# Performance work log

Hardware: AMD Instinct MI355X
Metric: run time of the kernel (lower is better)

The kernel has to match this reference:

```python
import jax, jax.numpy as jnp
import numpy as np

D_MODEL, N_HEADS, D_FF = 1024, 16, 4096
D_HEAD = D_MODEL // N_HEADS
B, S = 2, 2048
EPS = 1e-5


def setup_inputs() -> dict:
    key = jax.random.key(0)
    ks = jax.random.split(key, 12)
    sd = 1.0 / np.sqrt(D_MODEL)
    return {
        "x": jax.random.normal(ks[0], (B, S, D_MODEL), jnp.float32),
        "relative_bias": jax.random.normal(ks[1], (1, N_HEADS, S, S), jnp.float32),
        # attention projections, stored as (in, out) so y = x @ W
        "wq": jax.random.normal(ks[2], (D_MODEL, D_MODEL), jnp.float32) * sd,
        "wk": jax.random.normal(ks[3], (D_MODEL, D_MODEL), jnp.float32) * sd,
        "wv": jax.random.normal(ks[4], (D_MODEL, D_MODEL), jnp.float32) * sd,
        "wo": jax.random.normal(ks[5], (D_MODEL, D_MODEL), jnp.float32) * sd,
        "wo_b": jnp.zeros((D_MODEL,), jnp.float32),
        # FFN
        "w1": jax.random.normal(ks[6], (D_MODEL, D_FF), jnp.float32) * sd,
        "b1": jnp.zeros((D_FF,), jnp.float32),
        "w2": jax.random.normal(ks[7], (D_FF, D_MODEL), jnp.float32) * (1.0 / np.sqrt(D_FF)),
        "b2": jnp.zeros((D_MODEL,), jnp.float32),
        # LayerNorms
        "ln1_g": jnp.ones((D_MODEL,), jnp.float32),
        "ln1_b": jnp.zeros((D_MODEL,), jnp.float32),
        "ln2_g": jnp.ones((D_MODEL,), jnp.float32),
        "ln2_b": jnp.zeros((D_MODEL,), jnp.float32),
    }


def _layernorm(x, g, b):
    mu = jnp.mean(x, axis=-1, keepdims=True)
    var = jnp.mean(jnp.square(x - mu), axis=-1, keepdims=True)
    return (x - mu) * jax.lax.rsqrt(var + EPS) * g + b


def _attn(x, relative_bias, wq, wk, wv, wo, wo_b):
    b, s, d = x.shape
    # (B,S,D) -> (B,H,S,Dh)
    def split_heads(t):
        return t.reshape(b, s, N_HEADS, D_HEAD).transpose(0, 2, 1, 3)
    q = split_heads(x @ wq)
    k = split_heads(x @ wk)
    v = split_heads(x @ wv)
    scores = jnp.einsum("bhqd,bhkd->bhqk", q, k) / np.sqrt(D_HEAD) + relative_bias
    attn = jax.nn.softmax(scores, axis=-1)
    ctx = jnp.einsum("bhqk,bhkd->bhqd", attn, v)
    ctx = ctx.transpose(0, 2, 1, 3).reshape(b, s, d)
    return ctx @ wo + wo_b


def _ffn(x, w1, b1, w2, b2):
    return jax.nn.gelu(x @ w1 + b1, approximate=False) @ w2 + b2


def reference(x, relative_bias, wq, wk, wv, wo, wo_b, w1, b1, w2, b2,
              ln1_g, ln1_b, ln2_g, ln2_b):
    x = x + _attn(_layernorm(x, ln1_g, ln1_b), relative_bias, wq, wk, wv, wo, wo_b)
    x = x + _ffn(_layernorm(x, ln2_g, ln2_b), w1, b1, w2, b2)
    return x
```

## Files before the change

### kernel.cpp

```cpp
#include <hip/hip_runtime.h>
#include <hip/hip_bf16.h>
#include <stdint.h>

typedef unsigned short u16;
typedef __bf16 bf16x8 __attribute__((ext_vector_type(8)));
typedef u16   u16x8  __attribute__((ext_vector_type(8)));
typedef u16   u16x4  __attribute__((ext_vector_type(4)));
typedef float f32x4  __attribute__((ext_vector_type(4)));

__device__ __forceinline__ u16 f2bf(float f) {
  union { float f; uint32_t u; } v; v.f = f;
  uint32_t r = v.u + 0x7fffu + ((v.u >> 16) & 1u);
  return (u16)(r >> 16);
}

typedef __attribute__((address_space(1))) void gvoid_t;
typedef __attribute__((address_space(3))) void lvoid_t;
__device__ __forceinline__ void gload_lds16(const void* g, void* l) {
  __builtin_amdgcn_global_load_lds((gvoid_t*)g, (lvoid_t*)l, 16, 0, 0);
}

__global__ __launch_bounds__(256)
void ln_kernel(const float* __restrict__ x, const float* __restrict__ g,
               const float* __restrict__ b, u16* __restrict__ out) {
  const int row = blockIdx.x;
  const int tid = threadIdx.x;
  const float* xr = x + (size_t)row * 1024;
  f32x4 v = *(const f32x4*)&xr[tid * 4];
  float s = v[0] + v[1] + v[2] + v[3];
  float q = v[0]*v[0] + v[1]*v[1] + v[2]*v[2] + v[3]*v[3];
  #pragma unroll
  for (int o = 32; o > 0; o >>= 1) { s += __shfl_xor(s, o); q += __shfl_xor(q, o); }
  __shared__ float ss[4], qq[4];
  if ((tid & 63) == 0) { ss[tid >> 6] = s; qq[tid >> 6] = q; }
  __syncthreads();
  s = ss[0] + ss[1] + ss[2] + ss[3];
  q = qq[0] + qq[1] + qq[2] + qq[3];
  float mu = s * (1.0f / 1024.0f);
  float var = q * (1.0f / 1024.0f) - mu * mu;
  float rstd = rsqrtf(var + 1e-5f);
  u16x4 o4;
  #pragma unroll
  for (int i = 0; i < 4; ++i)
    o4[i] = f2bf((v[i] - mu) * rstd * g[tid * 4 + i] + b[tid * 4 + i]);
  *(u16x4*)&out[(size_t)row * 1024 + tid * 4] = o4;
}

__global__ __launch_bounds__(256)
void transpose_cast(const float* __restrict__ W, u16* __restrict__ Wt, int K, int N) {
  __shared__ float t[32][33];
  const int n0 = blockIdx.x * 32, k0 = blockIdx.y * 32;
  const int tx = threadIdx.x & 31, ty = threadIdx.x >> 5;
  #pragma unroll
  for (int i = 0; i < 4; ++i)
    t[ty + 8*i][tx] = W[(size_t)(k0 + ty + 8*i) * N + n0 + tx];
  __syncthreads();
  #pragma unroll
  for (int i = 0; i < 4; ++i)
    Wt[(size_t)(n0 + ty + 8*i) * K + k0 + tx] = f2bf(t[tx][ty + 8*i]);
}

template<int EPI>
__global__ __launch_bounds__(256, 2)
void gemm_bt(const u16* __restrict__ A, const u16* __restrict__ Bt,
             void* __restrict__ out, const float* __restrict__ bias,
             const float* __restrict__ resid, int M, int N, int K) {
  __shared__ u16 As[128 * 32];
  __shared__ u16 Bs[128 * 32];
  const int tid = threadIdx.x;
  const int w = tid >> 6, l = tid & 63;
  const int bm = blockIdx.x * 128, bn = blockIdx.y * 128;
  const int wr = (w >> 1) * 64, wc = (w & 1) * 64;
  const int l15 = l & 15, lhi = l >> 4;
  f32x4 acc[4][4] = {};

  const int r4 = tid >> 2;
  const int c8 = (tid & 3) * 8;
  const u16* ga0 = A  + (size_t)(bm + r4) * K + c8;
  const u16* ga1 = ga0 + (size_t)64 * K;
  const u16* gb0 = Bt + (size_t)(bn + r4) * K + c8;
  const u16* gb1 = gb0 + (size_t)64 * K;
  u16* lA0 = &As[(w * 16) * 32];
  u16* lA1 = &As[(64 + w * 16) * 32];
  u16* lB0 = &Bs[(w * 16) * 32];
  u16* lB1 = &Bs[(64 + w * 16) * 32];

  const int arow = (wr + l15) * 32 + lhi * 8;
  const int brow = (wc + l15) * 32 + lhi * 8;

  for (int k0 = 0; k0 < K; k0 += 32) {
    gload_lds16(ga0 + k0, lA0);
    gload_lds16(ga1 + k0, lA1);
    gload_lds16(gb0 + k0, lB0);
    gload_lds16(gb1 + k0, lB1);
    __syncthreads();
    bf16x8 a[4], b[4];
    #pragma unroll
    for (int m = 0; m < 4; ++m) a[m] = *(const bf16x8*)&As[arow + m * 16 * 32];
    #pragma unroll
    for (int n = 0; n < 4; ++n) b[n] = *(const bf16x8*)&Bs[brow + n * 16 * 32];
    #pragma unroll
    for (int m = 0; m < 4; ++m)
      #pragma unroll
      for (int n = 0; n < 4; ++n)
        acc[m][n] = __builtin_amdgcn_mfma_f32_16x16x32_bf16(a[m], b[n], acc[m][n], 0, 0, 0);
    __syncthreads();
  }

  #pragma unroll
  for (int m = 0; m < 4; ++m) {
    #pragma unroll
    for (int n = 0; n < 4; ++n) {
      #pragma unroll
      for (int r = 0; r < 4; ++r) {
        const int grow = bm + wr + m * 16 + lhi * 4 + r;
        const int gcol = bn + wc + n * 16 + l15;
        float vv = acc[m][n][r];
        if constexpr (EPI >= 1) vv += bias[gcol];
        if constexpr (EPI == 1) vv = 0.5f * vv * (1.0f + erff(vv * 0.70710678118f));
        if constexpr (EPI == 2) {
          vv += resid[(size_t)grow * N + gcol];
          ((float*)out)[(size_t)grow * N + gcol] = vv;
        } else {
          ((u16*)out)[(size_t)grow * N + gcol] = f2bf(vv);
        }
      }
    }
  }
}

__global__ __launch_bounds__(256, 2)
void attn_kernel(const u16* __restrict__ qkv, const float* __restrict__ bias,
                 u16* __restrict__ ctx) {
  const int qt = blockIdx.x;
  const int bh = blockIdx.y;
  const int b = bh >> 4, h = bh & 15;
  const int tid = threadIdx.x, w = tid >> 6, l = tid & 63;
  const int l15 = l & 15, lhi = l >> 4;
  const size_t ld = 3072;

  __shared__ u16 Kl[64 * 72];
  __shared__ u16 Vt[64 * 72];
  __shared__ u16 Pl[4][16 * 72];

  const u16* qp = qkv;
  const u16* kp = qkv + 1024;
  const u16* vp = qkv + 2048;

  bf16x8 qf[2];
  {
    const u16* qrow = qp + (size_t)(b * 2048 + qt * 64 + w * 16 + l15) * ld + h * 64 + lhi * 8;
    qf[0] = *(const bf16x8*)qrow;
    qf[1] = *(const bf16x8*)(qrow + 32);
  }

  float m_run[4] = {-1e30f, -1e30f, -1e30f, -1e30f};
  float s_run[4] = {0.f, 0.f, 0.f, 0.f};
  f32x4 octx[4] = {};

  const int key = tid & 63, dh = (tid >> 6) * 16;
  const u16* kgl = kp + (size_t)(b * 2048 + key) * ld + h * 64 + dh;
  const u16* vgl = vp + (size_t)(b * 2048 + key) * ld + h * 64 + dh;

  for (int kv0 = 0; kv0 < 2048; kv0 += 64) {
    u16x8 k0v = *(const u16x8*)(kgl + (size_t)kv0 * ld);
    u16x8 k1v = *(const u16x8*)(kgl + (size_t)kv0 * ld + 8);
    u16x8 v0v = *(const u16x8*)(vgl + (size_t)kv0 * ld);
    u16x8 v1v = *(const u16x8*)(vgl + (size_t)kv0 * ld + 8);
    *(u16x8*)&Kl[key * 72 + dh] = k0v;
    *(u16x8*)&Kl[key * 72 + dh + 8] = k1v;
    #pragma unroll
    for (int i = 0; i < 8; ++i) {
      Vt[(dh + i) * 72 + key]     = v0v[i];
      Vt[(dh + 8 + i) * 72 + key] = v1v[i];
    }
    __syncthreads();

    f32x4 sa[4] = {};
    #pragma unroll
    for (int nf = 0; nf < 4; ++nf) {
      bf16x8 kf0 = *(const bf16x8*)&Kl[(nf * 16 + l15) * 72 + lhi * 8];
      bf16x8 kf1 = *(const bf16x8*)&Kl[(nf * 16 + l15) * 72 + 32 + lhi * 8];
      sa[nf] = __builtin_amdgcn_mfma_f32_16x16x32_bf16(qf[0], kf0, sa[nf], 0, 0, 0);
      sa[nf] = __builtin_amdgcn_mfma_f32_16x16x32_bf16(qf[1], kf1, sa[nf], 0, 0, 0);
    }

    float sval[4][4];
    const size_t brow0 = (size_t)(h * 2048 + qt * 64 + w * 16 + lhi * 4) * 2048 + kv0 + l15;
    #pragma unroll
    for (int r = 0; r < 4; ++r)
      #pragma unroll
      for (int nf = 0; nf < 4; ++nf)
        sval[nf][r] = sa[nf][r] * 0.125f + bias[brow0 + (size_t)r * 2048 + nf * 16];

    #pragma unroll
    for (int r = 0; r < 4; ++r) {
      float mx = fmaxf(fmaxf(sval[0][r], sval[1][r]), fmaxf(sval[2][r], sval[3][r]));
      mx = fmaxf(mx, __shfl_xor(mx, 1));
      mx = fmaxf(mx, __shfl_xor(mx, 2));
      mx = fmaxf(mx, __shfl_xor(mx, 4));
      mx = fmaxf(mx, __shfl_xor(mx, 8));
      const float mnew = fmaxf(m_run[r], mx);
      const float fs = __expf(m_run[r] - mnew);
      s_run[r] *= fs;
      #pragma unroll
      for (int nf = 0; nf < 4; ++nf) octx[nf][r] *= fs;
      float ps = 0.f;
      #pragma unroll
      for (int nf = 0; nf < 4; ++nf) {
        float p = __expf(sval[nf][r] - mnew);
        sval[nf][r] = p;
        ps += p;
      }
      ps += __shfl_xor(ps, 1); ps += __shfl_xor(ps, 2);
      ps += __shfl_xor(ps, 4); ps += __shfl_xor(ps, 8);
      s_run[r] += ps;
      m_run[r] = mnew;
    }

    #pragma unroll
    for (int r = 0; r < 4; ++r)
      #pragma unroll
      for (int nf = 0; nf < 4; ++nf)
        Pl[w][(lhi * 4 + r) * 72 + nf * 16 + l15] = f2bf(sval[nf][r]);
    __syncthreads();

    #pragma unroll
    for (int ks = 0; ks < 2; ++ks) {
      bf16x8 pa = *(const bf16x8*)&Pl[w][l15 * 72 + ks * 32 + lhi * 8];
      #pragma unroll
      for (int nf = 0; nf < 4; ++nf) {
        bf16x8 bv = *(const bf16x8*)&Vt[(nf * 16 + l15) * 72 + ks * 32 + lhi * 8];
        octx[nf] = __builtin_amdgcn_mfma_f32_16x16x32_bf16(pa, bv, octx[nf], 0, 0, 0);
      }
    }
    __syncthreads();
  }

  #pragma unroll
  for (int nf = 0; nf < 4; ++nf)
    #pragma unroll
    for (int r = 0; r < 4; ++r) {
      const int grow = b * 2048 + qt * 64 + w * 16 + lhi * 4 + r;
      const int gcol = h * 64 + nf * 16 + l15;
      ctx[(size_t)grow * 1024 + gcol] = f2bf(octx[nf][r] / s_run[r]);
    }
}

extern "C" void kernel_launch(void* const* d_in, const int* in_sizes, int n_in,
                              void* d_out, int out_size, void* d_ws, size_t ws_size,
                              hipStream_t stream) {
  const float* x    = (const float*)d_in[0];
  const float* rb   = (const float*)d_in[1];
  const float* wq   = (const float*)d_in[2];
  const float* wk   = (const float*)d_in[3];
  const float* wv   = (const float*)d_in[4];
  const float* wo   = (const float*)d_in[5];
  const float* wo_b = (const float*)d_in[6];
  const float* w1   = (const float*)d_in[7];
  const float* b1   = (const float*)d_in[8];
  const float* w2   = (const float*)d_in[9];
  const float* b2   = (const float*)d_in[10];
  const float* ln1g = (const float*)d_in[11];
  const float* ln1b = (const float*)d_in[12];
  const float* ln2g = (const float*)d_in[13];
  const float* ln2b = (const float*)d_in[14];

  char* ws = (char*)d_ws;
  u16*   xn    = (u16*)(ws + 0);
  u16*   qkvb  = (u16*)(ws + (8u << 20));
  u16*   hbuf  = (u16*)(ws + (8u << 20));
  u16*   ctxb  = (u16*)(ws + (32u << 20));
  float* x1    = (float*)(ws + (40u << 20));
  u16*   wqkvt = (u16*)(ws + (56u << 20));
  u16*   wot   = (u16*)(ws + (62u << 20));
  u16*   w1t   = (u16*)(ws + (64u << 20));
  u16*   w2t   = (u16*)(ws + (72u << 20));

  transpose_cast<<<dim3(32, 32),  256, 0, stream>>>(wq, wqkvt,                 1024, 1024);
  transpose_cast<<<dim3(32, 32),  256, 0, stream>>>(wk, wqkvt + 1024 * 1024,   1024, 1024);
  transpose_cast<<<dim3(32, 32),  256, 0, stream>>>(wv, wqkvt + 2048 * 1024,   1024, 1024);
  transpose_cast<<<dim3(32, 32),  256, 0, stream>>>(wo, wot,                   1024, 1024);
  transpose_cast<<<dim3(128, 32), 256, 0, stream>>>(w1, w1t,                   1024, 4096);
  transpose_cast<<<dim3(32, 128), 256, 0, stream>>>(w2, w2t,                   4096, 1024);

  ln_kernel<<<4096, 256, 0, stream>>>(x, ln1g, ln1b, xn);
  gemm_bt<0><<<dim3(32, 24), 256, 0, stream>>>(xn, wqkvt, qkvb, nullptr, nullptr, 4096, 3072, 1024);
  attn_kernel<<<dim3(32, 32), 256, 0, stream>>>(qkvb, rb, ctxb);
  gemm_bt<2><<<dim3(32, 8), 256, 0, stream>>>(ctxb, wot, x1, wo_b, x, 4096, 1024, 1024);
  ln_kernel<<<4096, 256, 0, stream>>>(x1, ln2g, ln2b, xn);
  gemm_bt<1><<<dim3(32, 32), 256, 0, stream>>>(xn, w1t, hbuf, b1, nullptr, 4096, 4096, 1024);
  gemm_bt<2><<<dim3(32, 8), 256, 0, stream>>>(hbuf, w2t, (float*)d_out, b2, x1, 4096, 1024, 4096);

  (void)in_sizes; (void)n_in; (void)out_size; (void)ws_size;
}
```

Before: 424.6 us.

## Process both batches per attention block to share bias loads, prefetch K/V

```diff
diff --git a/kernel.cpp b/kernel.cpp
--- a/kernel.cpp
+++ b/kernel.cpp
@@ -133,118 +133,173 @@
 void attn_kernel(const u16* __restrict__ qkv, const float* __restrict__ bias,
                  u16* __restrict__ ctx) {
   const int qt = blockIdx.x;
-  const int bh = blockIdx.y;
-  const int b = bh >> 4, h = bh & 15;
+  const int h  = blockIdx.y;
   const int tid = threadIdx.x, w = tid >> 6, l = tid & 63;
   const int l15 = l & 15, lhi = l >> 4;
+  const int wb = w >> 1;
+  const int dc0 = (w & 1) * 32;
   const size_t ld = 3072;
-
-  __shared__ u16 Kl[64 * 72];
-  __shared__ u16 Vt[64 * 72];
+  const float LOG2E = 1.44269504f;
+
+  __shared__ u16 Kl[2][64 * 72];
+  __shared__ u16 Vt[2][64 * 72];
   __shared__ u16 Pl[4][16 * 72];
 
   const u16* qp = qkv;
   const u16* kp = qkv + 1024;
   const u16* vp = qkv + 2048;
 
-  bf16x8 qf[2];
+  bf16x8 qf[2][2];
+  #pragma unroll
+  for (int b = 0; b < 2; ++b) {
+    const u16* qrow = qp + (size_t)(b * 2048 + qt * 64 + w * 16 + l15) * ld + h * 64 + lhi * 8;
+    qf[b][0] = *(const bf16x8*)qrow;
+    qf[b][1] = *(const bf16x8*)(qrow + 32);
+  }
+
+  float m_run[2][4], s_run[2][4];
+  f32x4 octx[2][4] = {};
+  #pragma unroll
+  for (int b = 0; b < 2; ++b)
+    #pragma unroll
+    for (int r = 0; r < 4; ++r) { m_run[b][r] = -1e30f; s_run[b][r] = 0.f; }
+
+  const u16* kg0 = kp + (size_t)(wb * 2048 + l) * ld + h * 64 + dc0;
+  const u16* vg0 = vp + (size_t)(wb * 2048 + l) * ld + h * 64 + dc0;
+  const float* bg0 = bias + (size_t)(h * 2048 + qt * 64 + w * 16 + lhi * 4) * 2048 + l15;
+
+  u16x8 kpf[4], vpf[4];
+  float biasA[16], biasB[16];
+
+  #pragma unroll
+  for (int j = 0; j < 4; ++j) kpf[j] = *(const u16x8*)(kg0 + j * 8);
+  #pragma unroll
+  for (int j = 0; j < 4; ++j) vpf[j] = *(const u16x8*)(vg0 + j * 8);
+  #pragma unroll
+  for (int r = 0; r < 4; ++r)
+    #pragma unroll
+    for (int nf = 0; nf < 4; ++nf)
+      biasA[r * 4 + nf] = bg0[(size_t)r * 2048 + nf * 16] * LOG2E;
   {
-    const u16* qrow = qp + (size_t)(b * 2048 + qt * 64 + w * 16 + l15) * ld + h * 64 + lhi * 8;
-    qf[0] = *(const bf16x8*)qrow;
-    qf[1] = *(const bf16x8*)(qrow + 32);
-  }
-
-  float m_run[4] = {-1e30f, -1e30f, -1e30f, -1e30f};
-  float s_run[4] = {0.f, 0.f, 0.f, 0.f};
-  f32x4 octx[4] = {};
-
-  const int key = tid & 63, dh = (tid >> 6) * 16;
-  const u16* kgl = kp + (size_t)(b * 2048 + key) * ld + h * 64 + dh;
-  const u16* vgl = vp + (size_t)(b * 2048 + key) * ld + h * 64 + dh;
-
-  for (int kv0 = 0; kv0 < 2048; kv0 += 64) {
-    u16x8 k0v = *(const u16x8*)(kgl + (size_t)kv0 * ld);
-    u16x8 k1v = *(const u16x8*)(kgl + (size_t)kv0 * ld + 8);
-    u16x8 v0v = *(const u16x8*)(vgl + (size_t)kv0 * ld);
-    u16x8 v1v = *(const u16x8*)(vgl + (size_t)kv0 * ld + 8);
-    *(u16x8*)&Kl[key * 72 + dh] = k0v;
-    *(u16x8*)&Kl[key * 72 + dh + 8] = k1v;
-    #pragma unroll
-    for (int i = 0; i < 8; ++i) {
-      Vt[(dh + i) * 72 + key]     = v0v[i];
-      Vt[(dh + 8 + i) * 72 + key] = v1v[i];
+    u16* kd = &Kl[wb][l * 72 + dc0];
+    #pragma unroll
+    for (int j = 0; j < 4; ++j) *(u16x8*)(kd + j * 8) = kpf[j];
+    #pragma unroll
+    for (int j = 0; j < 4; ++j)
+      #pragma unroll
+      for (int i = 0; i < 8; ++i)
+        Vt[wb][(dc0 + j * 8 + i) * 72 + l] = vpf[j][i];
+  }
+  __syncthreads();
+
+  auto iter = [&](int it, float (&bcur)[16], float (&bnxt)[16]) {
+    const int kv0 = it * 64;
+    const bool pf = it < 31;
+    if (pf) {
+      const u16* kg = kg0 + (size_t)(kv0 + 64) * ld;
+      const u16* vg = vg0 + (size_t)(kv0 + 64) * ld;
+      #pragma unroll
+      for (int j = 0; j < 4; ++j) kpf[j] = *(const u16x8*)(kg + j * 8);
+      #pragma unroll
+      for (int j = 0; j < 4; ++j) vpf[j] = *(const u16x8*)(vg + j * 8);
+      #pragma unroll
+      for (int r = 0; r < 4; ++r)
+        #pragma unroll
+        for (int nf = 0; nf < 4; ++nf)
+          bnxt[r * 4 + nf] = bg0[(size_t)r * 2048 + kv0 + 64 + nf * 16] * LOG2E;
+    }
+    f32x4 sa[2][4] = {};
+    #pragma unroll
+    for (int b = 0; b < 2; ++b)
+      #pragma unroll
+      for (int nf = 0; nf < 4; ++nf) {
+        bf16x8 kf0 = *(const bf16x8*)&Kl[b][(nf * 16 + l15) * 72 + lhi * 8];
+        bf16x8 kf1 = *(const bf16x8*)&Kl[b][(nf * 16 + l15) * 72 + 32 + lhi * 8];
+        sa[b][nf] = __builtin_amdgcn_mfma_f32_16x16x32_bf16(qf[b][0], kf0, sa[b][nf], 0, 0, 0);
+        sa[b][nf] = __builtin_amdgcn_mfma_f32_16x16x32_bf16(qf[b][1], kf1, sa[b][nf], 0, 0, 0);
+      }
+    #pragma unroll
+    for (int b = 0; b < 2; ++b) {
+      float p[4][4];
+      #pragma unroll
+      for (int r = 0; r < 4; ++r)
+        #pragma unroll
+        for (int nf = 0; nf < 4; ++nf)
+          p[r][nf] = fmaf(sa[b][nf][r], 0.18033688f , bcur[r * 4 + nf]);
+      #pragma unroll
+      for (int r = 0; r < 4; ++r) {
+        float mx = fmaxf(fmaxf(p[r][0], p[r][1]), fmaxf(p[r][2], p[r][3]));
+        mx = fmaxf(mx, __shfl_xor(mx, 1));
+        mx = fmaxf(mx, __shfl_xor(mx, 2));
+        mx = fmaxf(mx, __shfl_xor(mx, 4));
+        mx = fmaxf(mx, __shfl_xor(mx, 8));
+        if (mx > m_run[b][r] + 8.0f) {
+          const float fs = exp2f(m_run[b][r] - mx);
+          s_run[b][r] *= fs;
+          #pragma unroll
+          for (int nf = 0; nf < 4; ++nf) octx[b][nf][r] *= fs;
+          m_run[b][r] = mx;
+        }
+        const float mm = m_run[b][r];
+        float ps = 0.f;
+        #pragma unroll
+        for (int nf = 0; nf < 4; ++nf) {
+          const float e = exp2f(p[r][nf] - mm);
+          p[r][nf] = e;
+          ps += e;
+        }
+        ps += __shfl_xor(ps, 1); ps += __shfl_xor(ps, 2);
+        ps += __shfl_xor(ps, 4); ps += __shfl_xor(ps, 8);
+        s_run[b][r] += ps;
+      }
+      #pragma unroll
+      for (int r = 0; r < 4; ++r)
+        #pragma unroll
+        for (int nf = 0; nf < 4; ++nf)
+          Pl[w][(lhi * 4 + r) * 72 + nf * 16 + l15] = f2bf(p[r][nf]);
+      #pragma unroll
+      for (int ks = 0; ks < 2; ++ks) {
+        bf16x8 pa = *(const bf16x8*)&Pl[w][l15 * 72 + ks * 32 + lhi * 8];
+        #pragma unroll
+        for (int nf = 0; nf < 4; ++nf) {
+          bf16x8 bv = *(const bf16x8*)&Vt[b][(nf * 16 + l15) * 72 + ks * 32 + lhi * 8];
+          octx[b][nf] = __builtin_amdgcn_mfma_f32_16x16x32_bf16(pa, bv, octx[b][nf], 0, 0, 0);
+        }
+      }
     }
     __syncthreads();
-
-    f32x4 sa[4] = {};
-    #pragma unroll
-    for (int nf = 0; nf < 4; ++nf) {
-      bf16x8 kf0 = *(const bf16x8*)&Kl[(nf * 16 + l15) * 72 + lhi * 8];
-      bf16x8 kf1 = *(const bf16x8*)&Kl[(nf * 16 + l15) * 72 + 32 + lhi * 8];
-      sa[nf] = __builtin_amdgcn_mfma_f32_16x16x32_bf16(qf[0], kf0, sa[nf], 0, 0, 0);
-      sa[nf] = __builtin_amdgcn_mfma_f32_16x16x32_bf16(qf[1], kf1, sa[nf], 0, 0, 0);
-    }
-
-    float sval[4][4];
-    const size_t brow0 = (size_t)(h * 2048 + qt * 64 + w * 16 + lhi * 4) * 2048 + kv0 + l15;
-    #pragma unroll
-    for (int r = 0; r < 4; ++r)
-      #pragma unroll
-      for (int nf = 0; nf < 4; ++nf)
-        sval[nf][r] = sa[nf][r] * 0.125f + bias[brow0 + (size_t)r * 2048 + nf * 16];
-
-    #pragma unroll
-    for (int r = 0; r < 4; ++r) {
-      float mx = fmaxf(fmaxf(sval[0][r], sval[1][r]), fmaxf(sval[2][r], sval[3][r]));
-      mx = fmaxf(mx, __shfl_xor(mx, 1));
-      mx = fmaxf(mx, __shfl_xor(mx, 2));
-      mx = fmaxf(mx, __shfl_xor(mx, 4));
-      mx = fmaxf(mx, __shfl_xor(mx, 8));
-      const float mnew = fmaxf(m_run[r], mx);
-      const float fs = __expf(m_run[r] - mnew);
-      s_run[r] *= fs;
-      #pragma unroll
-      for (int nf = 0; nf < 4; ++nf) octx[nf][r] *= fs;
-      float ps = 0.f;
-      #pragma unroll
-      for (int nf = 0; nf < 4; ++nf) {
-        float p = __expf(sval[nf][r] - mnew);
-        sval[nf][r] = p;
-        ps += p;
-      }
-      ps += __shfl_xor(ps, 1); ps += __shfl_xor(ps, 2);
-      ps += __shfl_xor(ps, 4); ps += __shfl_xor(ps, 8);
-      s_run[r] += ps;
-      m_run[r] = mnew;
-    }
-
-    #pragma unroll
-    for (int r = 0; r < 4; ++r)
-      #pragma unroll
-      for (int nf = 0; nf < 4; ++nf)
-        Pl[w][(lhi * 4 + r) * 72 + nf * 16 + l15] = f2bf(sval[nf][r]);
-    __syncthreads();
-
-    #pragma unroll
-    for (int ks = 0; ks < 2; ++ks) {
-      bf16x8 pa = *(const bf16x8*)&Pl[w][l15 * 72 + ks * 32 + lhi * 8];
-      #pragma unroll
-      for (int nf = 0; nf < 4; ++nf) {
-        bf16x8 bv = *(const bf16x8*)&Vt[(nf * 16 + l15) * 72 + ks * 32 + lhi * 8];
-        octx[nf] = __builtin_amdgcn_mfma_f32_16x16x32_bf16(pa, bv, octx[nf], 0, 0, 0);
-      }
+    if (pf) {
+      u16* kd = &Kl[wb][l * 72 + dc0];
+      #pragma unroll
+      for (int j = 0; j < 4; ++j) *(u16x8*)(kd + j * 8) = kpf[j];
+      #pragma unroll
+      for (int j = 0; j < 4; ++j)
+        #pragma unroll
+        for (int i = 0; i < 8; ++i)
+          Vt[wb][(dc0 + j * 8 + i) * 72 + l] = vpf[j][i];
     }
     __syncthreads();
-  }
-
-  #pragma unroll
-  for (int nf = 0; nf < 4; ++nf)
-    #pragma unroll
-    for (int r = 0; r < 4; ++r) {
-      const int grow = b * 2048 + qt * 64 + w * 16 + lhi * 4 + r;
-      const int gcol = h * 64 + nf * 16 + l15;
-      ctx[(size_t)grow * 1024 + gcol] = f2bf(octx[nf][r] / s_run[r]);
-    }
+  };
+
+  for (int it2 = 0; it2 < 16; ++it2) {
+    iter(2 * it2,     biasA, biasB);
+    iter(2 * it2 + 1, biasB, biasA);
+  }
+
+  #pragma unroll
+  for (int b = 0; b < 2; ++b) {
+    float inv[4];
+    #pragma unroll
+    for (int r = 0; r < 4; ++r) inv[r] = 1.0f / s_run[b][r];
+    #pragma unroll
+    for (int nf = 0; nf < 4; ++nf)
+      #pragma unroll
+      for (int r = 0; r < 4; ++r) {
+        const int grow = b * 2048 + qt * 64 + w * 16 + lhi * 4 + r;
+        const int gcol = h * 64 + nf * 16 + l15;
+        ctx[(size_t)grow * 1024 + gcol] = f2bf(octx[b][nf][r] * inv[r]);
+      }
+  }
 }
 
 extern "C" void kernel_launch(void* const* d_in, const int* in_sizes, int n_in,
@@ -286,7 +341,7 @@
 
   ln_kernel<<<4096, 256, 0, stream>>>(x, ln1g, ln1b, xn);
   gemm_bt<0><<<dim3(32, 24), 256, 0, stream>>>(xn, wqkvt, qkvb, nullptr, nullptr, 4096, 3072, 1024);
-  attn_kernel<<<dim3(32, 32), 256, 0, stream>>>(qkvb, rb, ctxb);
+  attn_kernel<<<dim3(32, 16), 256, 0, stream>>>(qkvb, rb, ctxb);
   gemm_bt<2><<<dim3(32, 8), 256, 0, stream>>>(ctxb, wot, x1, wo_b, x, 4096, 1024, 1024);
   ln_kernel<<<4096, 256, 0, stream>>>(x1, ln2g, ln2b, xn);
   gemm_bt<1><<<dim3(32, 32), 256, 0, stream>>>(xn, w1t, hbuf, b1, nullptr, 4096, 4096, 1024);
```

After: 445.2 us. 1.05x slower.

## Restructure attention to share bias across batches and prefetch K/V tiles

Applied to the files above, without the earlier changes.

```diff
diff --git a/kernel.cpp b/kernel.cpp
--- a/kernel.cpp
+++ b/kernel.cpp
@@ -18,6 +18,27 @@
 typedef __attribute__((address_space(3))) void lvoid_t;
 __device__ __forceinline__ void gload_lds16(const void* g, void* l) {
   __builtin_amdgcn_global_load_lds((gvoid_t*)g, (lvoid_t*)l, 16, 0, 0);
+}
+
+template<int CTRL>
+__device__ __forceinline__ float dpp_f(float x) {
+  int i = __builtin_bit_cast(int, x);
+  i = __builtin_amdgcn_update_dpp(i, i, CTRL, 0xF, 0xF, true);
+  return __builtin_bit_cast(float, i);
+}
+__device__ __forceinline__ float rowmax16(float x) {
+  x = fmaxf(x, dpp_f<0x128>(x));
+  x = fmaxf(x, dpp_f<0x124>(x));
+  x = fmaxf(x, dpp_f<0x122>(x));
+  x = fmaxf(x, dpp_f<0x121>(x));
+  return x;
+}
+__device__ __forceinline__ float rowsum16(float x) {
+  x += dpp_f<0x128>(x);
+  x += dpp_f<0x124>(x);
+  x += dpp_f<0x122>(x);
+  x += dpp_f<0x121>(x);
+  return x;
 }
 
 __global__ __launch_bounds__(256)
@@ -129,121 +150,171 @@
   }
 }
 
-__global__ __launch_bounds__(256, 2)
+#define SWZ(row) ((((row) & 7) ^ (((row) >> 3) & 7)) << 3)
+
+__global__ __launch_bounds__(256, 4)
 void attn_kernel(const u16* __restrict__ qkv, const float* __restrict__ bias,
                  u16* __restrict__ ctx) {
   const int qt = blockIdx.x;
-  const int bh = blockIdx.y;
-  const int b = bh >> 4, h = bh & 15;
+  const int h  = blockIdx.y;
   const int tid = threadIdx.x, w = tid >> 6, l = tid & 63;
   const int l15 = l & 15, lhi = l >> 4;
+  const int wb  = w >> 1;
+  const int qr0 = qt * 32 + (w & 1) * 16;
   const size_t ld = 3072;
 
-  __shared__ u16 Kl[64 * 72];
-  __shared__ u16 Vt[64 * 72];
-  __shared__ u16 Pl[4][16 * 72];
+  __shared__ u16 Kl[2][4096];
+  __shared__ u16 Vt[2][4096];
+  __shared__ u16 Pl[4][1024];
 
   const u16* qp = qkv;
   const u16* kp = qkv + 1024;
   const u16* vp = qkv + 2048;
 
-  bf16x8 qf[2];
+  const int sb = tid >> 7, t = tid & 127;
+  const int kg4 = (t >> 3) * 4, dg8 = (t & 7) * 8;
+  const u16* kbase = kp + ((size_t)sb * 2048 + kg4) * ld + h * 64 + dg8;
+  const u16* vbase = vp + ((size_t)sb * 2048 + kg4) * ld + h * 64 + dg8;
+
+  bf16x8 qf0, qf1;
   {
-    const u16* qrow = qp + (size_t)(b * 2048 + qt * 64 + w * 16 + l15) * ld + h * 64 + lhi * 8;
-    qf[0] = *(const bf16x8*)qrow;
-    qf[1] = *(const bf16x8*)(qrow + 32);
+    const u16* qrow = qp + ((size_t)wb * 2048 + qr0 + l15) * ld + h * 64 + lhi * 8;
+    qf0 = *(const bf16x8*)qrow;
+    qf1 = *(const bf16x8*)(qrow + 32);
   }
 
-  float m_run[4] = {-1e30f, -1e30f, -1e30f, -1e30f};
-  float s_run[4] = {0.f, 0.f, 0.f, 0.f};
+  const float* bg0 = bias + ((size_t)h * 2048 + qr0 + lhi * 4) * 2048 + l15;
+
+  float m_run[4], s_run[4];
   f32x4 octx[4] = {};
-
-  const int key = tid & 63, dh = (tid >> 6) * 16;
-  const u16* kgl = kp + (size_t)(b * 2048 + key) * ld + h * 64 + dh;
-  const u16* vgl = vp + (size_t)(b * 2048 + key) * ld + h * 64 + dh;
-
-  for (int kv0 = 0; kv0 < 2048; kv0 += 64) {
-    u16x8 k0v = *(const u16x8*)(kgl + (size_t)kv0 * ld);
-    u16x8 k1v = *(const u16x8*)(kgl + (size_t)kv0 * ld + 8);
-    u16x8 v0v = *(const u16x8*)(vgl + (size_t)kv0 * ld);
-    u16x8 v1v = *(const u16x8*)(vgl + (size_t)kv0 * ld + 8);
-    *(u16x8*)&Kl[key * 72 + dh] = k0v;
-    *(u16x8*)&Kl[key * 72 + dh + 8] = k1v;
+  #pragma unroll
+  for (int r = 0; r < 4; ++r) { m_run[r] = -1e30f; s_run[r] = 0.f; }
+
+  u16x8 kpf[4], vpf[4];
+  uint32_t bpkA[8], bpkB[8];
+
+  auto load_kv = [&](int kv) {
+    #pragma unroll
+    for (int j = 0; j < 4; ++j) kpf[j] = *(const u16x8*)(kbase + (size_t)(kv + j) * ld);
+    #pragma unroll
+    for (int j = 0; j < 4; ++j) vpf[j] = *(const u16x8*)(vbase + (size_t)(kv + j) * ld);
+  };
+  auto load_bias = [&](int kv, uint32_t (&bp)[8]) {
+    float bt[16];
+    #pragma unroll
+    for (int r = 0; r < 4; ++r)
+      #pragma unroll
+      for (int nf = 0; nf < 4; ++nf)
+        bt[r * 4 + nf] = bg0[(size_t)r * 2048 + kv + nf * 16] * 1.44269504f;
+    #pragma unroll
+    for (int k = 0; k < 8; ++k)
+      bp[k] = (uint32_t)f2bf(bt[2 * k]) | ((uint32_t)f2bf(bt[2 * k + 1]) << 16);
+  };
+  auto store_kv = [&]() {
+    #pragma unroll
+    for (int j = 0; j < 4; ++j) {
+      const int row = kg4 + j;
+      *(u16x8*)&Kl[sb][row * 64 + (dg8 ^ SWZ(row))] = kpf[j];
+    }
     #pragma unroll
     for (int i = 0; i < 8; ++i) {
-      Vt[(dh + i) * 72 + key]     = v0v[i];
-      Vt[(dh + 8 + i) * 72 + key] = v1v[i];
-    }
-    __syncthreads();
+      const int d = dg8 + i;
+      u16x4 vq = { vpf[0][i], vpf[1][i], vpf[2][i], vpf[3][i] };
+      *(u16x4*)&Vt[sb][d * 64 + (kg4 ^ SWZ(d))] = vq;
+    }
+  };
+
+  load_kv(0);
+  load_bias(0, bpkA);
+  store_kv();
+  __syncthreads();
+
+  auto iter = [&](int it, uint32_t (&bc)[8], uint32_t (&bn)[8]) {
+    const int kv0 = it * 64;
+    const bool pf = it < 31;
+    if (pf) { load_kv(kv0 + 64); load_bias(kv0 + 64, bn); }
 
     f32x4 sa[4] = {};
     #pragma unroll
     for (int nf = 0; nf < 4; ++nf) {
-      bf16x8 kf0 = *(const bf16x8*)&Kl[(nf * 16 + l15) * 72 + lhi * 8];
-      bf16x8 kf1 = *(const bf16x8*)&Kl[(nf * 16 + l15) * 72 + 32 + lhi * 8];
-      sa[nf] = __builtin_amdgcn_mfma_f32_16x16x32_bf16(qf[0], kf0, sa[nf], 0, 0, 0);
-      sa[nf] = __builtin_amdgcn_mfma_f32_16x16x32_bf16(qf[1], kf1, sa[nf], 0, 0, 0);
-    }
-
-    float sval[4][4];
-    const size_t brow0 = (size_t)(h * 2048 + qt * 64 + w * 16 + lhi * 4) * 2048 + kv0 + l15;
+      const int row = nf * 16 + l15;
+      const int s = SWZ(row);
+      bf16x8 kf0 = *(const bf16x8*)&Kl[wb][row * 64 + ((lhi * 8) ^ s)];
+      bf16x8 kf1 = *(const bf16x8*)&Kl[wb][row * 64 + ((32 + lhi * 8) ^ s)];
+      sa[nf] = __builtin_amdgcn_mfma_f32_16x16x32_bf16(qf0, kf0, sa[nf], 0, 0, 0);
+      sa[nf] = __builtin_amdgcn_mfma_f32_16x16x32_bf16(qf1, kf1, sa[nf], 0, 0, 0);
+    }
+
+    float bb[16];
+    #pragma unroll
+    for (int k = 0; k < 8; ++k) {
+      bb[2 * k]     = __builtin_bit_cast(float, bc[k] << 16);
+      bb[2 * k + 1] = __builtin_bit_cast(float, bc[k] & 0xffff0000u);
+    }
+    float p[4][4];
     #pragma unroll
     for (int r = 0; r < 4; ++r)
       #pragma unroll
       for (int nf = 0; nf < 4; ++nf)
-        sval[nf][r] = sa[nf][r] * 0.125f + bias[brow0 + (size_t)r * 2048 + nf * 16];
-
+        p[r][nf] = fmaf(sa[nf][r], 0.18033688f, bb[r * 4 + nf]);
     #pragma unroll
     for (int r = 0; r < 4; ++r) {
-      float mx = fmaxf(fmaxf(sval[0][r], sval[1][r]), fmaxf(sval[2][r], sval[3][r]));
-      mx = fmaxf(mx, __shfl_xor(mx, 1));
-      mx = fmaxf(mx, __shfl_xor(mx, 2));
-      mx = fmaxf(mx, __shfl_xor(mx, 4));
-      mx = fmaxf(mx, __shfl_xor(mx, 8));
-      const float mnew = fmaxf(m_run[r], mx);
-      const float fs = __expf(m_run[r] - mnew);
-      s_run[r] *= fs;
-      #pragma unroll
-      for (int nf = 0; nf < 4; ++nf) octx[nf][r] *= fs;
-      float ps = 0.f;
+      float mx = fmaxf(fmaxf(p[r][0], p[r][1]), fmaxf(p[r][2], p[r][3]));
+      mx = rowmax16(mx);
+      if (mx > m_run[r] + 8.0f) {
+        const float fs = exp2f(m_run[r] - mx);
+        s_run[r] *= fs;
+        #pragma unroll
+        for (int nf = 0; nf < 4; ++nf) octx[nf][r] *= fs;
+        m_run[r] = mx;
+      }
+      const float mm = m_run[r];
+      float e0 = exp2f(p[r][0] - mm), e1 = exp2f(p[r][1] - mm);
+      float e2 = exp2f(p[r][2] - mm), e3 = exp2f(p[r][3] - mm);
+      p[r][0] = e0; p[r][1] = e1; p[r][2] = e2; p[r][3] = e3;
+      s_run[r] += rowsum16((e0 + e1) + (e2 + e3));
+    }
+
+    #pragma unroll
+    for (int r = 0; r < 4; ++r) {
+      const int row = lhi * 4 + r;
+      const int s = SWZ(row);
+      #pragma unroll
+      for (int nf = 0; nf < 4; ++nf)
+        Pl[w][row * 64 + ((nf * 16 + l15) ^ s)] = f2bf(p[r][nf]);
+    }
+
+    #pragma unroll
+    for (int ks = 0; ks < 2; ++ks) {
+      bf16x8 pa = *(const bf16x8*)&Pl[w][l15 * 64 + ((ks * 32 + lhi * 8) ^ SWZ(l15))];
       #pragma unroll
       for (int nf = 0; nf < 4; ++nf) {
-        float p = __expf(sval[nf][r] - mnew);
-        sval[nf][r] = p;
-        ps += p;
-      }
-      ps += __shfl_xor(ps, 1); ps += __shfl_xor(ps, 2);
-      ps += __shfl_xor(ps, 4); ps += __shfl_xor(ps, 8);
-      s_run[r] += ps;
-      m_run[r] = mnew;
-    }
-
-    #pragma unroll
-    for (int r = 0; r < 4; ++r)
-      #pragma unroll
-      for (int nf = 0; nf < 4; ++nf)
-        Pl[w][(lhi * 4 + r) * 72 + nf * 16 + l15] = f2bf(sval[nf][r]);
-    __syncthreads();
-
-    #pragma unroll
-    for (int ks = 0; ks < 2; ++ks) {
-      bf16x8 pa = *(const bf16x8*)&Pl[w][l15 * 72 + ks * 32 + lhi * 8];
-      #pragma unroll
-      for (int nf = 0; nf < 4; ++nf) {
-        bf16x8 bv = *(const bf16x8*)&Vt[(nf * 16 + l15) * 72 + ks * 32 + lhi * 8];
+        const int row = nf * 16 + l15;
+        bf16x8 bv = *(const bf16x8*)&Vt[wb][row * 64 + ((ks * 32 + lhi * 8) ^ SWZ(row))];
         octx[nf] = __builtin_amdgcn_mfma_f32_16x16x32_bf16(pa, bv, octx[nf], 0, 0, 0);
       }
     }
+
     __syncthreads();
+    if (pf) store_kv();
+    __syncthreads();
+  };
+
+  for (int it2 = 0; it2 < 16; ++it2) {
+    iter(2 * it2,     bpkA, bpkB);
+    iter(2 * it2 + 1, bpkB, bpkA);
   }
 
+  float inv[4];
+  #pragma unroll
+  for (int r = 0; r < 4; ++r) inv[r] = 1.0f / s_run[r];
   #pragma unroll
   for (int nf = 0; nf < 4; ++nf)
     #pragma unroll
     for (int r = 0; r < 4; ++r) {
-      const int grow = b * 2048 + qt * 64 + w * 16 + lhi * 4 + r;
+      const int grow = wb * 2048 + qr0 + lhi * 4 + r;
       const int gcol = h * 64 + nf * 16 + l15;
-      ctx[(size_t)grow * 1024 + gcol] = f2bf(octx[nf][r] / s_run[r]);
+      ctx[(size_t)grow * 1024 + gcol] = f2bf(octx[nf][r] * inv[r]);
     }
 }
 
@@ -277,16 +348,16 @@
   u16*   w1t   = (u16*)(ws + (64u << 20));
   u16*   w2t   = (u16*)(ws + (72u << 20));
 
-  transpose_cast<<<dim3(32, 32),  256, 0, stream>>>(wq, wqkvt,                 1024, 1024);
-  transpose_cast<<<dim3(32, 32),  256, 0, stream>>>(wk, wqkvt + 1024 * 1024,   1024, 1024);
-  transpose_cast<<<dim3(32, 32),  256, 0, stream>>>(wv, wqkvt + 2048 * 1024,   1024, 1024);
-  transpose_cast<<<dim3(32, 32),  256, 0, stream>>>(wo, wot,                   1024, 1024);
-  transpose_cast<<<dim3(128, 32), 256, 0, stream>>>(w1, w1t,                   1024, 4096);
-  transpose_cast<<<dim3(32, 128), 256, 0, stream>>>(w2, w2t,                   4096, 1024);
+  transpose_cast<<<dim3(32, 32),  256, 0, stream>>>(wq, wqkvt,               1024, 1024);
+  transpose_cast<<<dim3(32, 32),  256, 0, stream>>>(wk, wqkvt + 1024 * 1024, 1024, 1024);
+  transpose_cast<<<dim3(32, 32),  256, 0, stream>>>(wv, wqkvt + 2048 * 1024, 1024, 1024);
+  transpose_cast<<<dim3(32, 32),  256, 0, stream>>>(wo, wot,                 1024, 1024);
+  transpose_cast<<<dim3(128, 32), 256, 0, stream>>>(w1, w1t,                 1024, 4096);
+  transpose_cast<<<dim3(32, 128), 256, 0, stream>>>(w2, w2t,                 4096, 1024);
 
   ln_kernel<<<4096, 256, 0, stream>>>(x, ln1g, ln1b, xn);
   gemm_bt<0><<<dim3(32, 24), 256, 0, stream>>>(xn, wqkvt, qkvb, nullptr, nullptr, 4096, 3072, 1024);
-  attn_kernel<<<dim3(32, 32), 256, 0, stream>>>(qkvb, rb, ctxb);
+  attn_kernel<<<dim3(64, 16), 256, 0, stream>>>(qkvb, rb, ctxb);
   gemm_bt<2><<<dim3(32, 8), 256, 0, stream>>>(ctxb, wot, x1, wo_b, x, 4096, 1024, 1024);
   ln_kernel<<<4096, 256, 0, stream>>>(x1, ln2g, ln2b, xn);
   gemm_bt<1><<<dim3(32, 32), 256, 0, stream>>>(xn, w1t, hbuf, b1, nullptr, 4096, 4096, 1024);
```

Result: slower. 752.4 us (+77.2%).
